# Kernel tuning notes

Measured on AMD Instinct MI355X. Metric: run time of the kernel, lower is better.

## Reference

```python
import jax, jax.numpy as jnp
import numpy as np

B, H, W = 32, 56, 56
C_IN, C_OUT, GROUPS, K = 256, 256, 32, 3
EPS = 1e-5


def setup_inputs() -> dict:
    key = jax.random.key(0)
    k1, k2 = jax.random.split(key, 2)
    x = jax.random.normal(k1, (B, H, W, C_IN), dtype=jnp.float32)
    # HWIO grouped-conv kernel: I = C_IN // GROUPS = 8; equivalent to the
    # concatenation of the 32 per-group [3,3,8,8] Conv2d kernels along O.
    w = jax.random.normal(k2, (K, K, C_IN // GROUPS, C_OUT), dtype=jnp.float32) * 0.05
    b = jnp.zeros((C_OUT,), dtype=jnp.float32)
    gamma = jnp.ones((C_OUT,), dtype=jnp.float32)
    beta = jnp.zeros((C_OUT,), dtype=jnp.float32)
    return {"x": x, "w": w, "b": b, "gamma": gamma, "beta": beta}


def reference(x, w, b, gamma, beta):
    # Grouped conv: same math as tf.split -> per-group Conv2d -> tf.concat,
    # expressed as one native grouped convolution (feature_group_count).
    y = jax.lax.conv_general_dilated(
        x, w,
        window_strides=(1, 1),
        padding="SAME",
        dimension_numbers=("NHWC", "HWIO", "NHWC"),
        feature_group_count=GROUPS,
    ) + b  # [B,H,W,C_OUT]
    # BatchNorm (training forward: batch statistics over N,H,W per channel)
    mean = jnp.mean(y, axis=(0, 1, 2))
    var = jnp.var(y, axis=(0, 1, 2))
    y = (y - mean) * jax.lax.rsqrt(var + EPS) * gamma + beta
    # Act('relu')
    return jax.nn.relu(y)
```

## Files before the change

### kernel.cpp

```cpp
#include <hip/hip_runtime.h>
#include <hip/hip_bf16.h>

#define BB 32
#define HH 56
#define WW 56
#define CC 256
#define NPIX (BB*HH*WW)
#define EPS 1e-5f

typedef short bf16x8 __attribute__((ext_vector_type(8)));
typedef float f32x4  __attribute__((ext_vector_type(4)));

__device__ __forceinline__ unsigned short f2bf(float f) {
    __hip_bfloat16 h = __float2bfloat16(f);
    return *reinterpret_cast<unsigned short*>(&h);
}


__global__ void k0_zero(float* stats) { stats[threadIdx.x] = 0.f; }

__global__ __launch_bounds__(256) void k1_conv(
    const float* __restrict__ x, const float* __restrict__ wgt,
    __hip_bfloat16* __restrict__ y, float* __restrict__ stats)
{
    __shared__ unsigned short xt[10*58*16];
    __shared__ unsigned short wb[16*160];
    __shared__ float bsum[16], bsq[16];

    const int gp = blockIdx.x;
    const int hb = blockIdx.y;
    const int b  = blockIdx.z;
    const int t  = threadIdx.x;
    const int h0 = hb * 8;

    if (t < 16) { bsum[t] = 0.f; bsq[t] = 0.f; }

    for (int i = t; i < 10*58*4; i += 256) {
        int ci4 = i & 3;
        int cq  = i >> 2;
        int col = cq % 58;
        int row = cq / 58;
        int hh  = h0 - 1 + row;
        int wc  = col - 1;
        float4 v = make_float4(0.f, 0.f, 0.f, 0.f);
        if ((unsigned)hh < HH && (unsigned)wc < WW)
            v = *(const float4*)(x + (((size_t)(b*HH + hh)*WW + wc)*CC + gp*16 + ci4*4));
        ushort4 s;
        s.x = f2bf(v.x); s.y = f2bf(v.y); s.z = f2bf(v.z); s.w = f2bf(v.w);
        *(ushort4*)(xt + (row*58 + col)*16 + ci4*4) = s;
    }

    for (int i = t; i < 16*160; i += 256) {
        int n  = i / 160;
        int kk = i - n*160;
        int g  = kk >= 80;
        int r  = kk - g*80;
        int tap = r >> 3;
        int ci  = r & 7;
        unsigned short val = 0;
        if (tap < 9 && (n >> 3) == g)
            val = f2bf(wgt[(tap*8 + ci)*CC + gp*16 + n]);
        wb[i] = val;
    }
    __syncthreads();

    const int lane = t & 63;
    const int rp   = t >> 6;
    const int n    = lane & 15;
    const int q    = lane >> 4;
    const int m    = lane & 15;
    const int rowr = rp*2 + (m >> 3);
    const int colb = m & 7;

    bf16x8 bfrag[5];
    #pragma unroll
    for (int s = 0; s < 5; ++s)
        bfrag[s] = *(const bf16x8*)(wb + n*160 + s*32 + q*8);

    int aoff[5];
    #pragma unroll
    for (int s = 0; s < 5; ++s) {
        int o  = s*4 + q;
        int g  = (o >= 10);
        int tp = o - g*10;
        if (tp == 9) tp = 0;
        int dh = tp / 3, dw = tp - dh*3;
        aoff[s] = ((rowr + 1 - 1 + dh)*58 + colb + dw)*16 + g*8;
    }

    const int hq = q >> 1;
    const int wq = (q & 1) * 4;
    float lsum = 0.f, lsq = 0.f;

    for (int ct = 0; ct < 7; ++ct) {
        f32x4 acc = {0.f, 0.f, 0.f, 0.f};
        #pragma unroll
        for (int s = 0; s < 5; ++s) {
            bf16x8 af = *(const bf16x8*)(xt + aoff[s] + ct*128);
            acc = __builtin_amdgcn_mfma_f32_16x16x32_bf16(af, bfrag[s], acc, 0, 0, 0);
        }
        const int h = h0 + rp*2 + hq;
        const size_t base = (((size_t)(b*HH + h))*WW + ct*8 + wq)*CC + gp*16 + n;
        #pragma unroll
        for (int i = 0; i < 4; ++i) {
            float v = acc[i];
            y[base + (size_t)i*CC] = __float2bfloat16(v);
            lsum += v;
            lsq  += v * v;
        }
    }

    atomicAdd(&bsum[n], lsum);
    atomicAdd(&bsq[n],  lsq);
    __syncthreads();
    if (t < 16) {
        atomicAdd(&stats[gp*16 + t],       bsum[t]);
        atomicAdd(&stats[256 + gp*16 + t], bsq[t]);
    }
}

__global__ void k2_finalize(const float* __restrict__ stats,
                            const float* __restrict__ gamma,
                            const float* __restrict__ beta,
                            float* __restrict__ ss)
{
    int c = threadIdx.x;
    float inv_n = 1.f / (float)NPIX;
    float mean = stats[c] * inv_n;
    float var  = stats[256 + c] * inv_n - mean * mean;
    float scale = gamma[c] * rsqrtf(var + EPS);
    ss[c]       = scale;
    ss[256 + c] = beta[c] - mean * scale;
}

__global__ __launch_bounds__(256) void k3_norm(
    const __hip_bfloat16* __restrict__ y, const float* __restrict__ ss,
    float* __restrict__ out)
{
    const int t   = threadIdx.x;
    const int oct = t & 31;
    const int pr  = t >> 5;
    const int c0  = oct * 8;

    float4 sc0 = *(const float4*)(ss + c0);
    float4 sc1 = *(const float4*)(ss + c0 + 4);
    float4 sh0 = *(const float4*)(ss + 256 + c0);
    float4 sh1 = *(const float4*)(ss + 256 + c0 + 4);

    const uint4* yv = (const uint4*)y;
    float4* ov = (float4*)out;
    const int px0 = blockIdx.x * 128 + pr;

    #pragma unroll
    for (int i = 0; i < 16; ++i) {
        const int px = px0 + i*8;
        uint4 d = yv[(size_t)px*32 + oct];

        float f0 = __uint_as_float((d.x & 0xffffu) << 16);
        float f1 = __uint_as_float(d.x & 0xffff0000u);
        float f2 = __uint_as_float((d.y & 0xffffu) << 16);
        float f3 = __uint_as_float(d.y & 0xffff0000u);
        float f4 = __uint_as_float((d.z & 0xffffu) << 16);
        float f5 = __uint_as_float(d.z & 0xffff0000u);
        float f6 = __uint_as_float((d.w & 0xffffu) << 16);
        float f7 = __uint_as_float(d.w & 0xffff0000u);

        float4 o0, o1;
        o0.x = fmaxf(0.f, f0 * sc0.x + sh0.x);
        o0.y = fmaxf(0.f, f1 * sc0.y + sh0.y);
        o0.z = fmaxf(0.f, f2 * sc0.z + sh0.z);
        o0.w = fmaxf(0.f, f3 * sc0.w + sh0.w);
        o1.x = fmaxf(0.f, f4 * sc1.x + sh1.x);
        o1.y = fmaxf(0.f, f5 * sc1.y + sh1.y);
        o1.z = fmaxf(0.f, f6 * sc1.z + sh1.z);
        o1.w = fmaxf(0.f, f7 * sc1.w + sh1.w);

        ov[(size_t)px*64 + oct*2]     = o0;
        ov[(size_t)px*64 + oct*2 + 1] = o1;
    }
}

extern "C" void kernel_launch(void* const* d_in, const int* in_sizes, int n_in,
                              void* d_out, int out_size, void* d_ws, size_t ws_size,
                              hipStream_t stream) {
    const float* x     = (const float*)d_in[0];
    const float* wgt   = (const float*)d_in[1];
    const float* gamma = (const float*)d_in[3];
    const float* beta  = (const float*)d_in[4];
    float* out = (float*)d_out;

    float* stats = (float*)d_ws;
    float* ss    = (float*)((char*)d_ws + 2048);
    __hip_bfloat16* y = (__hip_bfloat16*)((char*)d_ws + 4096);

    k0_zero<<<1, 512, 0, stream>>>(stats);
    k1_conv<<<dim3(16, 7, BB), 256, 0, stream>>>(x, wgt, y, stats);
    k2_finalize<<<1, 256, 0, stream>>>(stats, gamma, beta, ss);
    k3_norm<<<NPIX/128, 256, 0, stream>>>(y, ss, out);
}
```

Before: 258.2 us.

## Batch conv input loads, pad LDS tile stride, shrink norm blocks

```diff
diff --git a/kernel.cpp b/kernel.cpp
--- a/kernel.cpp
+++ b/kernel.cpp
@@ -23,7 +23,7 @@
     const float* __restrict__ x, const float* __restrict__ wgt,
     __hip_bfloat16* __restrict__ y, float* __restrict__ stats)
 {
-    __shared__ unsigned short xt[10*58*16];
+    __shared__ unsigned short xt[10*58*24];
     __shared__ unsigned short wb[16*160];
     __shared__ float bsum[16], bsq[16];
 
@@ -35,32 +35,45 @@
 
     if (t < 16) { bsum[t] = 0.f; bsq[t] = 0.f; }
 
-    for (int i = t; i < 10*58*4; i += 256) {
-        int ci4 = i & 3;
-        int cq  = i >> 2;
-        int col = cq % 58;
-        int row = cq / 58;
-        int hh  = h0 - 1 + row;
-        int wc  = col - 1;
-        float4 v = make_float4(0.f, 0.f, 0.f, 0.f);
-        if ((unsigned)hh < HH && (unsigned)wc < WW)
-            v = *(const float4*)(x + (((size_t)(b*HH + hh)*WW + wc)*CC + gp*16 + ci4*4));
-        ushort4 s;
-        s.x = f2bf(v.x); s.y = f2bf(v.y); s.z = f2bf(v.z); s.w = f2bf(v.w);
-        *(ushort4*)(xt + (row*58 + col)*16 + ci4*4) = s;
-    }
-
-    for (int i = t; i < 16*160; i += 256) {
-        int n  = i / 160;
-        int kk = i - n*160;
-        int g  = kk >= 80;
-        int r  = kk - g*80;
-        int tap = r >> 3;
-        int ci  = r & 7;
-        unsigned short val = 0;
-        if (tap < 9 && (n >> 3) == g)
-            val = f2bf(wgt[(tap*8 + ci)*CC + gp*16 + n]);
-        wb[i] = val;
+    float4 v[10];
+    int    off[10];
+    #pragma unroll
+    for (int j = 0; j < 10; ++j) {
+        const int i   = j*256 + t;
+        const int ci4 = i & 3;
+        const int cq  = i >> 2;
+        const int row = cq / 58;
+        const int col = cq - row*58;
+        const int hh  = h0 - 1 + row;
+        const int wc  = col - 1;
+        off[j] = (row*58 + col)*24 + ci4*4;
+        v[j] = make_float4(0.f, 0.f, 0.f, 0.f);
+        if (i < 2320 && (unsigned)hh < HH && (unsigned)wc < WW)
+            v[j] = *(const float4*)(x + (((size_t)(b*HH + hh)*WW + wc)*CC + gp*16 + ci4*4));
+    }
+    {
+        const int n  = t >> 4;
+        const int k0 = t & 15;
+        #pragma unroll
+        for (int j = 0; j < 10; ++j) {
+            const int kk  = k0 + j*16;
+            const int g   = (kk >= 80);
+            const int r   = kk - g*80;
+            const int tap = r >> 3, ci = r & 7;
+            unsigned short val = 0;
+            if (tap < 9 && (n >> 3) == g)
+                val = f2bf(wgt[(tap*8 + ci)*CC + gp*16 + n]);
+            wb[n*160 + kk] = val;
+        }
+    }
+    #pragma unroll
+    for (int j = 0; j < 10; ++j) {
+        if (j*256 + t < 2320) {
+            ushort4 s;
+            s.x = f2bf(v[j].x); s.y = f2bf(v[j].y);
+            s.z = f2bf(v[j].z); s.w = f2bf(v[j].w);
+            *(ushort4*)(xt + off[j]) = s;
+        }
     }
     __syncthreads();
 
@@ -85,28 +98,29 @@
         int tp = o - g*10;
         if (tp == 9) tp = 0;
         int dh = tp / 3, dw = tp - dh*3;
-        aoff[s] = ((rowr + 1 - 1 + dh)*58 + colb + dw)*16 + g*8;
+        aoff[s] = ((rowr + dh)*58 + colb + dw)*24 + g*8;
     }
 
     const int hq = q >> 1;
     const int wq = (q & 1) * 4;
     float lsum = 0.f, lsq = 0.f;
 
+    #pragma unroll 2
     for (int ct = 0; ct < 7; ++ct) {
         f32x4 acc = {0.f, 0.f, 0.f, 0.f};
         #pragma unroll
         for (int s = 0; s < 5; ++s) {
-            bf16x8 af = *(const bf16x8*)(xt + aoff[s] + ct*128);
+            bf16x8 af = *(const bf16x8*)(xt + aoff[s] + ct*192);
             acc = __builtin_amdgcn_mfma_f32_16x16x32_bf16(af, bfrag[s], acc, 0, 0, 0);
         }
         const int h = h0 + rp*2 + hq;
         const size_t base = (((size_t)(b*HH + h))*WW + ct*8 + wq)*CC + gp*16 + n;
         #pragma unroll
         for (int i = 0; i < 4; ++i) {
-            float v = acc[i];
-            y[base + (size_t)i*CC] = __float2bfloat16(v);
-            lsum += v;
-            lsq  += v * v;
+            float vv = acc[i];
+            y[base + (size_t)i*CC] = __float2bfloat16(vv);
+            lsum += vv;
+            lsq  += vv * vv;
         }
     }
 
@@ -149,21 +163,24 @@
 
     const uint4* yv = (const uint4*)y;
     float4* ov = (float4*)out;
-    const int px0 = blockIdx.x * 128 + pr;
-
-    #pragma unroll
-    for (int i = 0; i < 16; ++i) {
+    const int px0 = blockIdx.x * 32 + pr;
+
+    uint4 d[4];
+    #pragma unroll
+    for (int i = 0; i < 4; ++i)
+        d[i] = yv[(size_t)(px0 + i*8)*32 + oct];
+
+    #pragma unroll
+    for (int i = 0; i < 4; ++i) {
         const int px = px0 + i*8;
-        uint4 d = yv[(size_t)px*32 + oct];
-
-        float f0 = __uint_as_float((d.x & 0xffffu) << 16);
-        float f1 = __uint_as_float(d.x & 0xffff0000u);
-        float f2 = __uint_as_float((d.y & 0xffffu) << 16);
-        float f3 = __uint_as_float(d.y & 0xffff0000u);
-        float f4 = __uint_as_float((d.z & 0xffffu) << 16);
-        float f5 = __uint_as_float(d.z & 0xffff0000u);
-        float f6 = __uint_as_float((d.w & 0xffffu) << 16);
-        float f7 = __uint_as_float(d.w & 0xffff0000u);
+        float f0 = __uint_as_float((d[i].x & 0xffffu) << 16);
+        float f1 = __uint_as_float(d[i].x & 0xffff0000u);
+        float f2 = __uint_as_float((d[i].y & 0xffffu) << 16);
+        float f3 = __uint_as_float(d[i].y & 0xffff0000u);
+        float f4 = __uint_as_float((d[i].z & 0xffffu) << 16);
+        float f5 = __uint_as_float(d[i].z & 0xffff0000u);
+        float f6 = __uint_as_float((d[i].w & 0xffffu) << 16);
+        float f7 = __uint_as_float(d[i].w & 0xffff0000u);
 
         float4 o0, o1;
         o0.x = fmaxf(0.f, f0 * sc0.x + sh0.x);
@@ -196,5 +213,5 @@
     k0_zero<<<1, 512, 0, stream>>>(stats);
     k1_conv<<<dim3(16, 7, BB), 256, 0, stream>>>(x, wgt, y, stats);
     k2_finalize<<<1, 256, 0, stream>>>(stats, gamma, beta, ss);
-    k3_norm<<<NPIX/128, 256, 0, stream>>>(y, ss, out);
-}
+    k3_norm<<<NPIX/32, 256, 0, stream>>>(y, ss, out);
+}
```

Result: faster. 250.0 us (-3.2%).
